# Kernel optimization log

Measured on AMD Instinct MI355X. Metric: run time of the kernel, lower is better.

## Reference

```python
import jax, jax.numpy as jnp
import numpy as np

GRID = (128, 128, 128)
CENTER = (0.0, 0.0, 0.0)
SIZE = (400.0, 400.0, 400.0)
KERNEL_WIDTH = float(np.sqrt(3.0 * 3.0 * np.pi))  # ~5.317 (from module source)
SIGMA = KERNEL_WIDTH / 2.0
W = 2  # transverse window half-width in voxels (kernel_width / voxel_size ~ 1.7)
ROTATIONS = {'x': [1, 2, 0], 'y': [0, 2, 1], 'z': [0, 1, 2]}
N_LORS = 200000


def _make_lors(key, n, axis, half):
    # endpoints: main-axis coords pinned to the two FOV faces, transverse uniform
    u = jax.random.uniform(key, (n, 6), minval=-half, maxval=half, dtype=jnp.float32)
    u = u.at[:, axis].set(-half).at[:, axis + 3].set(half)
    return u


def setup_inputs() -> dict:
    key = jax.random.key(0)
    k0, k1, k2, k3 = jax.random.split(key, 4)
    image = jax.random.uniform(k0, GRID, dtype=jnp.float32)
    half = SIZE[0] / 2.0
    return {
        'image': image,
        'xlors': _make_lors(k1, N_LORS, 0, half),
        'ylors': _make_lors(k2, N_LORS, 1, half),
        'zlors': _make_lors(k3, N_LORS, 2, half),
    }


def _project_axis(image, lors, perm):
    # rotate image / geometry so the LOR main axis is the last (slice) axis
    img = jnp.transpose(image, perm)                      # [gx, gy, gz]
    g = [GRID[i] for i in perm]
    c = [CENTER[i] for i in perm]
    s = [SIZE[i] for i in perm]
    dx, dy, dz = s[0] / g[0], s[1] / g[1], s[2] / g[2]
    xmin, ymin, zmin = c[0] - s[0] / 2, c[1] - s[1] / 2, c[2] - s[2] / 2

    p0 = lors[:, jnp.array(perm)]                          # [N,3]
    p1 = lors[:, jnp.array([i + 3 for i in perm])]         # [N,3]
    dvec = p1 - p0
    L = jnp.sqrt(jnp.sum(dvec * dvec, axis=1))             # LOR length
    dzl = dvec[:, 2]
    path = dz * L / jnp.abs(dzl)                           # path length per slice

    di = jnp.arange(-W, W + 1)
    doff = jnp.stack(jnp.meshgrid(di, di, indexing='ij'), -1).reshape(-1, 2)  # [25,2]

    def step(acc, k):
        zc = zmin + (k.astype(jnp.float32) + 0.5) * dz     # slice-plane center
        t = (zc - p0[:, 2]) / dzl                          # [N] line parameter
        xc = p0[:, 0] + t * dvec[:, 0]
        yc = p0[:, 1] + t * dvec[:, 1]
        i0 = jnp.floor((xc - xmin) / dx).astype(jnp.int32)
        j0 = jnp.floor((yc - ymin) / dy).astype(jnp.int32)
        ii = i0[:, None] + doff[None, :, 0]                # [N,25]
        jj = j0[:, None] + doff[None, :, 1]
        xi = xmin + (ii.astype(jnp.float32) + 0.5) * dx
        yj = ymin + (jj.astype(jnp.float32) + 0.5) * dy
        d2 = (xi - xc[:, None]) ** 2 + (yj - yc[:, None]) ** 2
        w = jnp.exp(-d2 / (2.0 * SIGMA * SIGMA))
        w = w * (d2 <= KERNEL_WIDTH * KERNEL_WIDTH).astype(jnp.float32)
        inb = ((ii >= 0) & (ii < g[0]) & (jj >= 0) & (jj < g[1])).astype(jnp.float32)
        valid = ((t >= 0.0) & (t <= 1.0)).astype(jnp.float32)
        sl = jax.lax.dynamic_index_in_dim(img, k, axis=2, keepdims=False)  # [gx,gy]
        vals = sl[jnp.clip(ii, 0, g[0] - 1), jnp.clip(jj, 0, g[1] - 1)]
        contrib = jnp.sum(w * inb * vals, axis=1) * path * valid
        return acc + contrib, None

    acc, _ = jax.lax.scan(step, jnp.zeros(lors.shape[0], jnp.float32), jnp.arange(g[2]))
    return acc


def reference(image, xlors, ylors, zlors):
    px = _project_axis(image, xlors, ROTATIONS['x'])
    py = _project_axis(image, ylors, ROTATIONS['y'])
    pz = _project_axis(image, zlors, ROTATIONS['z'])
    return jnp.stack([px, py, pz])  # [3, N]
```

## Files before the change

### kernel.cpp

```cpp
#include <hip/hip_runtime.h>
#include <math.h>

constexpr float DXC    = 3.125f;
constexpr float INV_DX = 0.32f;
constexpr float XMINC  = -200.0f;
constexpr float KW2    = 9.0f * 3.14159265358979323846f;
constexpr float DXC2   = DXC * DXC;
constexpr float KW2C   = KW2 / DXC2;
constexpr float NEGL2C = -(2.0f / KW2) * 1.4426950408889634f * DXC2;
constexpr float WOFF   = 1.7983f;

constexpr int TPB    = 1024;
constexpr int LPB    = 1024;
constexpr int KSPLIT = 8;
constexpr int KCH    = 128 / KSPLIT;
constexpr int QTAB   = 1024;

__device__ inline unsigned bf16_rn(float x) {
    unsigned u = __float_as_uint(x);
    return (u + 0x7fffu + ((u >> 16) & 1u)) >> 16;
}
__device__ inline unsigned pk_bf16(float x, float y) {
    return bf16_rn(x) | (bf16_rn(y) << 16);
}
__device__ inline float uaf(unsigned u) { return __uint_as_float(u); }

__global__ __launch_bounds__(256) void prep_kernel(const float* __restrict__ img,
                                                   ushort* __restrict__ V0,
                                                   ushort* __restrict__ V1,
                                                   ushort* __restrict__ V2) {
    int o = blockIdx.x * 256 + threadIdx.x;
    float x = img[o];
    unsigned h = bf16_rn(x);
    V0[o] = (ushort)h;
    int c = o & 127, b = (o >> 7) & 127, a = o >> 14;
    V1[(b << 14) | (a << 7) | c] = (ushort)h;
    int j = o & 127, i = (o >> 7) & 127, k = o >> 14;
    V2[o] = (ushort)bf16_rn(img[(i << 14) | (j << 7) | k]);
}

__global__ __launch_bounds__(1024) void zero_kernel(float* __restrict__ out, int m) {
    int i = blockIdx.x * 1024 + threadIdx.x;
    if (i < m) out[i] = 0.0f;
}

__device__ inline void stage_one(const ushort* __restrict__ V, int k, int tid, void* dst) {
    const char* src = (const char*)(V + ((size_t)k << 14));
    char* d = (char*)dst;
    int wbase = (tid >> 6) << 10;
    int lane16 = (tid & 63) << 4;
#pragma unroll
    for (int c = 0; c < 2; ++c) {
        int half = c << 14;
        __builtin_amdgcn_global_load_lds(
            (__attribute__((address_space(1))) void*)(const_cast<char*>(src + half + wbase + lane16)),
            (__attribute__((address_space(3))) void*)(d + half + wbase),
            16, 0, 0);
    }
}

template <int AXIS>
__device__ inline void stage_issue(const float* __restrict__ img, int k, int tid,
                                   float4 st[4]) {
#pragma unroll
    for (int c = 0; c < 4; ++c) {
        int f4 = tid + TPB * c;
        int fl = f4 << 2;
        if (AXIS == 2) {
            int i = fl >> 7, j = fl & 127;
            const float* p = img + (i << 14) + (j << 7) + k;
            st[c] = make_float4(p[0], p[128], p[256], p[384]);
        } else {
            int off;
            if (AXIS == 1) off = ((fl >> 7) << 14) | (k << 7) | (fl & 127);
            else           off = (k << 14) | fl;
            st[c] = *reinterpret_cast<const float4*>(img + off);
        }
    }
}

__device__ inline void stage_write(const float4 st[4], ushort* slb, int tid) {
    uint* w = reinterpret_cast<uint*>(slb);
#pragma unroll
    for (int c = 0; c < 4; ++c) {
        int f4 = tid + TPB * c;
        w[f4 * 2]     = pk_bf16(st[c].x, st[c].y);
        w[f4 * 2 + 1] = pk_bf16(st[c].z, st[c].w);
    }
}

template <int AXIS, bool PRE>
__device__ void proj_axis(ushort (*sl)[16384], float4* wtab,
                          const ushort* __restrict__ V,
                          const float*  __restrict__ imgF,
                          const float*  __restrict__ lors,
                          float* __restrict__ out, int n, int blk, int ks)
{
    const int tid = threadIdx.x;
    const int lor = blk * LPB + tid;
    const bool active = lor < n;
    const int lorc = active ? lor : n - 1;

    const float* l = lors + (size_t)lorc * 6;
    float l0 = l[0], l1 = l[1], l2 = l[2], l3 = l[3], l4 = l[4], l5 = l[5];
    float p0x, p0y, p0z, p1x, p1y, p1z;
    if (AXIS == 0)      { p0x = l1; p0y = l2; p0z = l0; p1x = l4; p1y = l5; p1z = l3; }
    else if (AXIS == 1) { p0x = l0; p0y = l2; p0z = l1; p1x = l3; p1y = l5; p1z = l4; }
    else                { p0x = l0; p0y = l1; p0z = l2; p1x = l3; p1y = l4; p1z = l5; }

    float dvx = p1x - p0x, dvy = p1y - p0y, dvz = p1z - p0z;
    float L     = sqrtf(dvx * dvx + dvy * dvy + dvz * dvz);
    float pathL = DXC * L / fabsf(dvz);
    float invdz = 1.0f / dvz;

    float dux  = dvx * INV_DX, ux0 = (p0x - XMINC) * INV_DX;
    float dvyS = dvy * INV_DX, vy0 = (p0y - XMINC) * INV_DX;
    float tzs = invdz, tz0 = -p0z * invdz;

    const int k0 = ks * KCH, k1 = k0 + KCH;

    float dt = DXC * tzs;
    float cu = dux * dt, cv = dvyS * dt;
    float zc0 = fmaf((float)k0, DXC, XMINC + 0.5f * DXC);
    float t0  = fmaf(zc0, tzs, tz0);
    float u   = fmaf(t0, dux, ux0);
    float v   = fmaf(t0, dvyS, vy0);
    float acc = 0.0f;

    if (PRE) {
        stage_one(V, k0, tid, sl[k0 & 1]);
    } else {
        float4 st[4];
        stage_issue<AXIS>(imgF, k0, tid, st);
        stage_write(st, sl[k0 & 1], tid);
    }
    {
        float s = ((float)tid + 0.5f) * (4.0f / (float)QTAB);
        float4 e;
        float o0 = 0.5f - s, o1 = 1.5f - s, o2 = 2.5f - s, o3 = 3.5f - s;
        e.x = exp2f(o0 * o0 * NEGL2C);
        e.y = exp2f(o1 * o1 * NEGL2C);
        e.z = exp2f(o2 * o2 * NEGL2C);
        e.w = exp2f(o3 * o3 * NEGL2C);
        wtab[tid] = e;
    }
    __syncthreads();

    for (int k = k0; k < k1; ++k) {
        const ushort* sbuf = sl[k & 1];
        float4 st2[4];
        if (k < k1 - 1) {
            if (PRE) stage_one(V, k + 1, tid, sl[(k & 1) ^ 1]);
            else     stage_issue<AXIS>(imgF, k + 1, tid, st2);
        }

        float e0f = __builtin_amdgcn_fmed3f(floorf(v - WOFF), 0.0f, 124.0f);
        int   e0  = (int)e0f;
        int   qv  = (int)((v - e0f) * (QTAB / 4.0f));
        float4 eb = wtab[qv];
        float db0 = e0f + 0.5f - v;
        float b0 = db0 * db0;
        float gb = fmaf(2.0f, db0, 1.0f);
        float b1 = b0 + gb, gb1 = gb + 2.0f;
        float b2 = b1 + gb1, gb2 = gb1 + 2.0f;
        float b3 = b2 + gb2;

        float i0f = __builtin_amdgcn_fmed3f(floorf(u - WOFF), 0.0f, 124.0f);
        int   i0c = (int)i0f;
        int   qu  = (int)((u - i0f) * (QTAB / 4.0f));
        float4 ea = wtab[qu];
        float da0 = i0f + 0.5f - u;
        float a0 = da0 * da0;
        float ga = fmaf(2.0f, da0, 1.0f);
        float a1 = a0 + ga, ga1 = ga + 2.0f;
        float a2 = a1 + ga1, ga2 = ga1 + 2.0f;
        float a3 = a2 + ga2;
        float thr[4] = {KW2C - a0, KW2C - a1, KW2C - a2, KW2C - a3};
        float eaa[4] = {ea.x, ea.y, ea.z, ea.w};

        const uint* s32 = reinterpret_cast<const uint*>(sbuf);
        int dwc = e0 >> 1;
        int sh  = (e0 & 1) << 4;
        int rowdw = (i0c << 6) + dwc;
#pragma unroll
        for (int r = 0; r < 4; ++r) {
            const uint* sr = s32 + rowdw + (r << 6);
            uint d0 = sr[0], d1 = sr[1], d2 = sr[2];
            uint p01 = __builtin_amdgcn_alignbit(d1, d0, sh);
            uint p23 = __builtin_amdgcn_alignbit(d2, d1, sh);
            float w0 = uaf(p01 << 16);
            float w1 = uaf(p01 & 0xffff0000u);
            float w2 = uaf(p23 << 16);
            float w3 = uaf(p23 & 0xffff0000u);
            float tr = thr[r];
            float rs;
            rs = __fmul_rn((b0 <= tr) ? eb.x : 0.0f, w0);
            rs = fmaf((b1 <= tr) ? eb.y : 0.0f, w1, rs);
            rs = fmaf((b2 <= tr) ? eb.z : 0.0f, w2, rs);
            rs = fmaf((b3 <= tr) ? eb.w : 0.0f, w3, rs);
            acc = fmaf(eaa[r], rs, acc);
        }

        u += cu; v += cv;

        if (k < k1 - 1) {
            if (!PRE) stage_write(st2, sl[(k & 1) ^ 1], tid);
            __syncthreads();
        }
    }

    if (active) atomicAdd(out + lor, acc * pathL);
}

template <bool PRE>
__global__ __launch_bounds__(TPB, 8) void proj_fused(const float* __restrict__ img,
                                                     const ushort* __restrict__ V0,
                                                     const ushort* __restrict__ V1,
                                                     const ushort* __restrict__ V2,
                                                     const float* __restrict__ xl,
                                                     const float* __restrict__ yl,
                                                     const float* __restrict__ zl,
                                                     float* __restrict__ out,
                                                     int n, int nblk)
{
    __shared__ ushort sl[2][16384];
    __shared__ float4 wtab[QTAB];
    int per = nblk * KSPLIT;
    int axis = blockIdx.x / per;
    int r = blockIdx.x - axis * per;
    int blk = r >> 3;
    int ks  = r & 7;
    if (axis == 0)      proj_axis<0, PRE>(sl, wtab, V0, img, xl, out, n, blk, ks);
    else if (axis == 1) proj_axis<1, PRE>(sl, wtab, V1, img, yl, out + n, n, blk, ks);
    else                proj_axis<2, PRE>(sl, wtab, V2, img, zl, out + 2 * (size_t)n, n, blk, ks);
}

extern "C" void kernel_launch(void* const* d_in, const int* in_sizes, int n_in,
                              void* d_out, int out_size, void* d_ws, size_t ws_size,
                              hipStream_t stream) {
    const float* img   = (const float*)d_in[0];
    const float* xlors = (const float*)d_in[1];
    const float* ylors = (const float*)d_in[2];
    const float* zlors = (const float*)d_in[3];
    float* out = (float*)d_out;

    int n = in_sizes[1] / 6;
    int nblk = (n + LPB - 1) / LPB;
    int m = 3 * n;

    zero_kernel<<<(m + 1023) / 1024, 1024, 0, stream>>>(out, m);

    constexpr size_t VOL = 128 * 128 * 128;
    bool pre = ws_size >= 3 * VOL * sizeof(ushort);
    int grid = 3 * nblk * KSPLIT;

    if (pre) {
        ushort* V0 = (ushort*)d_ws;
        ushort* V1 = V0 + VOL;
        ushort* V2 = V1 + VOL;
        prep_kernel<<<VOL / 256, 256, 0, stream>>>(img, V0, V1, V2);
        proj_fused<true><<<grid, TPB, 0, stream>>>(img, V0, V1, V2,
                                                   xlors, ylors, zlors, out, n, nblk);
    } else {
        proj_fused<false><<<grid, TPB, 0, stream>>>(img, nullptr, nullptr, nullptr,
                                                    xlors, ylors, zlors, out, n, nblk);
    }
}
```

Baseline: 312.3 us.

## Switch slice storage to fp16 and precompute next-slice window before barrier

```diff
diff --git a/kernel.cpp b/kernel.cpp
--- a/kernel.cpp
+++ b/kernel.cpp
@@ -6,9 +6,9 @@
 constexpr float XMINC  = -200.0f;
 constexpr float KW2    = 9.0f * 3.14159265358979323846f;
 constexpr float DXC2   = DXC * DXC;
-constexpr float KW2C   = KW2 / DXC2;
 constexpr float NEGL2C = -(2.0f / KW2) * 1.4426950408889634f * DXC2;
 constexpr float WOFF   = 1.7983f;
+constexpr float WMIN   = 0.13533528323661270f;
 
 constexpr int TPB    = 1024;
 constexpr int LPB    = 1024;
@@ -16,14 +16,18 @@
 constexpr int KCH    = 128 / KSPLIT;
 constexpr int QTAB   = 1024;
 
-__device__ inline unsigned bf16_rn(float x) {
-    unsigned u = __float_as_uint(x);
-    return (u + 0x7fffu + ((u >> 16) & 1u)) >> 16;
-}
-__device__ inline unsigned pk_bf16(float x, float y) {
-    return bf16_rn(x) | (bf16_rn(y) << 16);
-}
-__device__ inline float uaf(unsigned u) { return __uint_as_float(u); }
+typedef __fp16 half2_t __attribute__((ext_vector_type(2)));
+
+__device__ inline ushort f16_rn(float x) {
+    union { __fp16 h; ushort u; } cv;
+    cv.h = (__fp16)x;
+    return cv.u;
+}
+__device__ inline uint pk_f16(float x, float y) {
+    union { half2_t h; uint u; } cv;
+    cv.h = __builtin_amdgcn_cvt_pkrtz(x, y);
+    return cv.u;
+}
 
 __global__ __launch_bounds__(256) void prep_kernel(const float* __restrict__ img,
                                                    ushort* __restrict__ V0,
@@ -31,12 +35,12 @@
                                                    ushort* __restrict__ V2) {
     int o = blockIdx.x * 256 + threadIdx.x;
     float x = img[o];
-    unsigned h = bf16_rn(x);
-    V0[o] = (ushort)h;
+    ushort h = f16_rn(x);
+    V0[o] = h;
     int c = o & 127, b = (o >> 7) & 127, a = o >> 14;
-    V1[(b << 14) | (a << 7) | c] = (ushort)h;
+    V1[(b << 14) | (a << 7) | c] = h;
     int j = o & 127, i = (o >> 7) & 127, k = o >> 14;
-    V2[o] = (ushort)bf16_rn(img[(i << 14) | (j << 7) | k]);
+    V2[o] = f16_rn(img[(i << 14) | (j << 7) | k]);
 }
 
 __global__ __launch_bounds__(1024) void zero_kernel(float* __restrict__ out, int m) {
@@ -84,9 +88,52 @@
 #pragma unroll
     for (int c = 0; c < 4; ++c) {
         int f4 = tid + TPB * c;
-        w[f4 * 2]     = pk_bf16(st[c].x, st[c].y);
-        w[f4 * 2 + 1] = pk_bf16(st[c].z, st[c].w);
-    }
+        w[f4 * 2]     = pk_f16(st[c].x, st[c].y);
+        w[f4 * 2 + 1] = pk_f16(st[c].z, st[c].w);
+    }
+}
+
+struct WIN { float4 ea, eb; int rowdw, sh; };
+
+__device__ inline WIN mkwin(float u, float v, const float4* wt) {
+    WIN w;
+    float e0f = __builtin_amdgcn_fmed3f(floorf(v - WOFF), 0.0f, 124.0f);
+    float i0f = __builtin_amdgcn_fmed3f(floorf(u - WOFF), 0.0f, 124.0f);
+    int qv = (int)((v - e0f) * (QTAB / 4.0f));
+    int qu = (int)((u - i0f) * (QTAB / 4.0f));
+    w.eb = wt[qv];
+    w.ea = wt[qu];
+    int e0 = (int)e0f, i0 = (int)i0f;
+    w.sh    = (e0 & 1) << 4;
+    w.rowdw = (i0 << 6) + (e0 >> 1);
+    return w;
+}
+
+__device__ inline float do_slice(const WIN& w, const uint* __restrict__ s32, float acc) {
+    float eaa[4] = {w.ea.x, w.ea.y, w.ea.z, w.ea.w};
+#pragma unroll
+    for (int r = 0; r < 4; ++r) {
+        const uint* sr = s32 + w.rowdw + (r << 6);
+        uint d0 = sr[0], d1 = sr[1], d2 = sr[2];
+        uint p01 = __builtin_amdgcn_alignbit(d1, d0, w.sh);
+        uint p23 = __builtin_amdgcn_alignbit(d2, d1, w.sh);
+        float er = eaa[r];
+        float g0 = er * w.eb.x, g1 = er * w.eb.y, g2 = er * w.eb.z, g3 = er * w.eb.w;
+        g0 = (g0 >= WMIN) ? g0 : 0.0f;
+        g1 = (g1 >= WMIN) ? g1 : 0.0f;
+        g2 = (g2 >= WMIN) ? g2 : 0.0f;
+        g3 = (g3 >= WMIN) ? g3 : 0.0f;
+        union { uint u; half2_t h; } a01, a23;
+        a01.u = p01; a23.u = p23;
+        float x0 = (float)a01.h.x, x1 = (float)a01.h.y;
+        float x2 = (float)a23.h.x, x3 = (float)a23.h.y;
+        float rs = __fmul_rn(g0, x0);
+        rs = fmaf(g1, x1, rs);
+        rs = fmaf(g2, x2, rs);
+        rs = fmaf(g3, x3, rs);
+        acc += rs;
+    }
+    return acc;
 }
 
 template <int AXIS, bool PRE>
@@ -146,6 +193,8 @@
     }
     __syncthreads();
 
+    WIN w = mkwin(u, v, wtab);
+
     for (int k = k0; k < k1; ++k) {
         const ushort* sbuf = sl[k & 1];
         float4 st2[4];
@@ -154,56 +203,11 @@
             else     stage_issue<AXIS>(imgF, k + 1, tid, st2);
         }
 
-        float e0f = __builtin_amdgcn_fmed3f(floorf(v - WOFF), 0.0f, 124.0f);
-        int   e0  = (int)e0f;
-        int   qv  = (int)((v - e0f) * (QTAB / 4.0f));
-        float4 eb = wtab[qv];
-        float db0 = e0f + 0.5f - v;
-        float b0 = db0 * db0;
-        float gb = fmaf(2.0f, db0, 1.0f);
-        float b1 = b0 + gb, gb1 = gb + 2.0f;
-        float b2 = b1 + gb1, gb2 = gb1 + 2.0f;
-        float b3 = b2 + gb2;
-
-        float i0f = __builtin_amdgcn_fmed3f(floorf(u - WOFF), 0.0f, 124.0f);
-        int   i0c = (int)i0f;
-        int   qu  = (int)((u - i0f) * (QTAB / 4.0f));
-        float4 ea = wtab[qu];
-        float da0 = i0f + 0.5f - u;
-        float a0 = da0 * da0;
-        float ga = fmaf(2.0f, da0, 1.0f);
-        float a1 = a0 + ga, ga1 = ga + 2.0f;
-        float a2 = a1 + ga1, ga2 = ga1 + 2.0f;
-        float a3 = a2 + ga2;
-        float thr[4] = {KW2C - a0, KW2C - a1, KW2C - a2, KW2C - a3};
-        float eaa[4] = {ea.x, ea.y, ea.z, ea.w};
-
-        const uint* s32 = reinterpret_cast<const uint*>(sbuf);
-        int dwc = e0 >> 1;
-        int sh  = (e0 & 1) << 4;
-        int rowdw = (i0c << 6) + dwc;
-#pragma unroll
-        for (int r = 0; r < 4; ++r) {
-            const uint* sr = s32 + rowdw + (r << 6);
-            uint d0 = sr[0], d1 = sr[1], d2 = sr[2];
-            uint p01 = __builtin_amdgcn_alignbit(d1, d0, sh);
-            uint p23 = __builtin_amdgcn_alignbit(d2, d1, sh);
-            float w0 = uaf(p01 << 16);
-            float w1 = uaf(p01 & 0xffff0000u);
-            float w2 = uaf(p23 << 16);
-            float w3 = uaf(p23 & 0xffff0000u);
-            float tr = thr[r];
-            float rs;
-            rs = __fmul_rn((b0 <= tr) ? eb.x : 0.0f, w0);
-            rs = fmaf((b1 <= tr) ? eb.y : 0.0f, w1, rs);
-            rs = fmaf((b2 <= tr) ? eb.z : 0.0f, w2, rs);
-            rs = fmaf((b3 <= tr) ? eb.w : 0.0f, w3, rs);
-            acc = fmaf(eaa[r], rs, acc);
-        }
+        acc = do_slice(w, reinterpret_cast<const uint*>(sbuf), acc);
 
         u += cu; v += cv;
-
         if (k < k1 - 1) {
+            w = mkwin(u, v, wtab);
             if (!PRE) stage_write(st2, sl[(k & 1) ^ 1], tid);
             __syncthreads();
         }
```

After: 314.7 us. Within noise of the previous version (+0.8%).
